# Kernel optimization log

Hardware: AMD Instinct MI355X
Metric: run time of the kernel (lower is better)

Reference implementation:

```python
import jax, jax.numpy as jnp
import numpy as np

K = 7          # neighborhood kernel size (7x7)
NH = 8         # num heads


def _nbr_idx(n):
    # NATTEN-style clamped windows: window start = clip(i - K//2, 0, n-K)
    pos = jnp.arange(n)
    start = jnp.clip(pos - K // 2, 0, n - K)          # (n,)
    idx = start[:, None] + jnp.arange(K)[None, :]     # (n, K) absolute key positions
    rel = idx - pos[:, None] + (K - 1)                # (n, K) in [0, 2K-2] for rpb lookup
    return idx, rel


def _forward(x, w_qkv, b_qkv, rpb, w_proj, b_proj, w_fc1, b_fc1, w_fc2, b_fc2):
    B, C, H, W = x.shape
    hd = C // NH
    scale = hd ** -0.5

    # ---- neighborhood attention (norm0 = Identity) ----
    xp = jnp.transpose(x, (0, 2, 3, 1))                           # (B,H,W,C)
    qkv = xp @ w_qkv + b_qkv                                      # (B,H,W,3C)
    qkv = qkv.reshape(B, H, W, 3, NH, hd)
    q = qkv[:, :, :, 0] * scale                                   # (B,H,W,nh,hd)
    k = qkv[:, :, :, 1]
    v = qkv[:, :, :, 2]

    idx_h, rel_h = _nbr_idx(H)                                    # (H,K)
    idx_w, rel_w = _nbr_idx(W)                                    # (W,K)

    # gather 7x7 neighborhoods: (B,H,K,W,K,nh,hd)
    k_nbr = k[:, idx_h][:, :, :, idx_w]
    v_nbr = v[:, idx_h][:, :, :, idx_w]

    # attention logits: (B,H,W,nh,K,K)
    attn = jnp.einsum('bxynd,bxiyjnd->bxynij', q, k_nbr)
    # relative positional bias: rpb (nh, 2K-1, 2K-1) -> (nh,H,K,W,K)
    bias = rpb[:, rel_h][:, :, :, rel_w]                          # (nh,H,K,W,K)
    attn = attn + jnp.transpose(bias, (1, 3, 0, 2, 4))[None]      # (B,H,W,nh,K,K)

    attn = jax.nn.softmax(attn.reshape(B, H, W, NH, K * K), axis=-1)
    attn = attn.reshape(B, H, W, NH, K, K)

    out = jnp.einsum('bxynij,bxiyjnd->bxynd', attn, v_nbr)        # (B,H,W,nh,hd)
    out = out.reshape(B, H, W, C) @ w_proj + b_proj               # (B,H,W,C)
    x1 = jnp.transpose(out, (0, 3, 1, 2)) + x                     # residual skip0

    # ---- MLP (1x1-conv style, channels-first; norm1 = Identity) ----
    h = jnp.einsum('bchw,cf->bfhw', x1, w_fc1) + b_fc1[None, :, None, None]
    h = jax.nn.gelu(h, approximate=False)                         # torch nn.GELU (erf)
    y = jnp.einsum('bfhw,fc->bchw', h, w_fc2) + b_fc2[None, :, None, None]
    return y + x1                                                 # residual skip1


def setup_inputs() -> dict:
    key = jax.random.key(0)
    B, C, H, W = 1, 256, 64, 128
    hid = int(C * 2.0)
    ks = jax.random.split(key, 8)
    s = 0.02
    return {
        'x': jax.random.normal(ks[0], (B, C, H, W), jnp.float32),
        'w_qkv': jax.random.normal(ks[1], (C, 3 * C), jnp.float32) * s,
        'b_qkv': jnp.zeros((3 * C,), jnp.float32),
        'rpb': jax.random.normal(ks[2], (NH, 2 * K - 1, 2 * K - 1), jnp.float32) * s,
        'w_proj': jax.random.normal(ks[3], (C, C), jnp.float32) * s,
        'b_proj': jnp.zeros((C,), jnp.float32),
        'w_fc1': jax.random.normal(ks[4], (C, hid), jnp.float32) * s,
        'b_fc1': jnp.zeros((hid,), jnp.float32),
        'w_fc2': jax.random.normal(ks[5], (hid, C), jnp.float32) * s,
        'b_fc2': jnp.zeros((C,), jnp.float32),
    }


def reference(x, w_qkv, b_qkv, rpb, w_proj, b_proj, w_fc1, b_fc1, w_fc2, b_fc2):
    return _forward(x, w_qkv, b_qkv, rpb, w_proj, b_proj, w_fc1, b_fc1, w_fc2, b_fc2)
```

## Files before the change

### kernel.cpp

```cpp
#include <hip/hip_runtime.h>

typedef unsigned short ushort;
typedef short bf16x8 __attribute__((ext_vector_type(8)));
typedef float f32x4 __attribute__((ext_vector_type(4)));

static __device__ __forceinline__ ushort f2b(float f) {
  unsigned u = __builtin_bit_cast(unsigned, f);
  u = (u + 0x7fffu + ((u >> 16) & 1u)) >> 16;
  return (ushort)u;
}
static __device__ __forceinline__ float b2f(ushort b) {
  return __builtin_bit_cast(float, (unsigned)b << 16);
}

static __device__ __forceinline__ void gll16(const ushort* g, ushort* l) {
  __builtin_amdgcn_global_load_lds(
      (const __attribute__((address_space(1))) void*)g,
      (__attribute__((address_space(3))) void*)l, 16, 0, 0);
}

__global__ __launch_bounds__(256) void prep_kernel(
    const float* __restrict__ x,
    const float* __restrict__ w_qkv, const float* __restrict__ w_proj,
    const float* __restrict__ w_fc1, const float* __restrict__ w_fc2,
    ushort* __restrict__ xb, ushort* __restrict__ wqkvT,
    ushort* __restrict__ wprojT, ushort* __restrict__ wfc1T,
    ushort* __restrict__ wfc2T)
{
  __shared__ float tile[32][33];
  int t = blockIdx.x;
  const float* src; ushort* dst; int R, Nc, r0, c0;
  if (t < 2048)              { src = x;      dst = xb;     R = 256; Nc = 8192; r0 = (t >> 8) * 32; c0 = (t & 255) * 32; }
  else if ((t -= 2048) < 192){ src = w_qkv;  dst = wqkvT;  R = 256; Nc = 768;  r0 = (t / 24) * 32; c0 = (t % 24) * 32; }
  else if ((t -= 192) < 64)  { src = w_proj; dst = wprojT; R = 256; Nc = 256;  r0 = (t / 8) * 32;  c0 = (t % 8) * 32; }
  else if ((t -= 64) < 128)  { src = w_fc1;  dst = wfc1T;  R = 256; Nc = 512;  r0 = (t / 16) * 32; c0 = (t % 16) * 32; }
  else           { t -= 128;   src = w_fc2;  dst = wfc2T;  R = 512; Nc = 256;  r0 = (t / 8) * 32;  c0 = (t % 8) * 32; }

  const int tx = threadIdx.x & 31, ty = threadIdx.x >> 5;
  #pragma unroll
  for (int i = 0; i < 4; i++)
    tile[ty + i * 8][tx] = src[(size_t)(r0 + ty + i * 8) * Nc + c0 + tx];
  __syncthreads();
  #pragma unroll
  for (int i = 0; i < 4; i++)
    dst[(size_t)(c0 + ty + i * 8) * R + r0 + tx] = f2b(tile[tx][ty + i * 8]);
}

template<int EPI, int KD>
__global__ __launch_bounds__(256) void gemm_mfma(
    const ushort* __restrict__ A, const ushort* __restrict__ Bt,
    const float* __restrict__ bias, const float* __restrict__ R,
    const ushort* __restrict__ RS,
    void* __restrict__ C0, void* __restrict__ C1,
    int M, int N)
{
  __shared__ __attribute__((aligned(16))) ushort As[64 * 128];
  __shared__ __attribute__((aligned(16))) ushort Bs[64 * 128];

  const int bm = blockIdx.y * 64;
  const int bn = blockIdx.x * 64;
  const int t  = threadIdx.x;
  const int w    = t >> 6;
  const int lane = t & 63;
  const int wm = (w & 1) * 32;
  const int wn = (w >> 1) * 32;
  const int lm = lane & 15;
  const int kq = lane >> 4;

  const int rl  = lane >> 4;
  const int cbx = (lane & 15) << 4;
  const int xr  = (lm & 7) << 4;

  f32x4 acc[2][2] = {};

  #pragma unroll
  for (int k0 = 0; k0 < KD; k0 += 128) {
    #pragma unroll
    for (int s = 0; s < 4; s++) {
      const int c = w * 4 + s;
      const int r = c * 4 + rl;
      const int off = (cbx ^ ((r & 7) << 4)) >> 1;
      gll16(A  + (size_t)(bm + r) * KD + k0 + off, As + c * 512);
      gll16(Bt + (size_t)(bn + r) * KD + k0 + off, Bs + c * 512);
    }
    __syncthreads();

    #pragma unroll
    for (int ks = 0; ks < 4; ks++) {
      const int kb = ks * 64 + (kq << 4);
      const int cs = kb ^ xr;
      bf16x8 a0 = *(const bf16x8*)((const char*)As + (wm + lm)      * 256 + cs);
      bf16x8 a1 = *(const bf16x8*)((const char*)As + (wm + 16 + lm) * 256 + cs);
      bf16x8 b0 = *(const bf16x8*)((const char*)Bs + (wn + lm)      * 256 + cs);
      bf16x8 b1 = *(const bf16x8*)((const char*)Bs + (wn + 16 + lm) * 256 + cs);
      acc[0][0] = __builtin_amdgcn_mfma_f32_16x16x32_bf16(a0, b0, acc[0][0], 0, 0, 0);
      acc[0][1] = __builtin_amdgcn_mfma_f32_16x16x32_bf16(a0, b1, acc[0][1], 0, 0, 0);
      acc[1][0] = __builtin_amdgcn_mfma_f32_16x16x32_bf16(a1, b0, acc[1][0], 0, 0, 0);
      acc[1][1] = __builtin_amdgcn_mfma_f32_16x16x32_bf16(a1, b1, acc[1][1], 0, 0, 0);
    }
    __syncthreads();
  }

  #pragma unroll
  for (int ti = 0; ti < 2; ti++) {
    #pragma unroll
    for (int tj = 0; tj < 2; tj++) {
      const int n  = bn + wn + tj * 16 + lm;
      const int m0 = bm + wm + ti * 16 + kq * 4;
      if (EPI == 3) {
        float4 v;
        float* vp = &v.x;
        #pragma unroll
        for (int r = 0; r < 4; r++)
          vp[r] = acc[ti][tj][r] + bias[n] + b2f(RS[(size_t)(m0 + r) * 256 + n]);
        *(float4*)((float*)C0 + (size_t)n * M + m0) = v;
      } else if (EPI == 0) {
        if (n < 512) {
          #pragma unroll
          for (int r = 0; r < 4; r++)
            ((ushort*)C0)[(size_t)(m0 + r) * N + n] = f2b(acc[ti][tj][r] + bias[n]);
        } else {
          ushort4 st;
          st.x = f2b(acc[ti][tj][0] + bias[n]);
          st.y = f2b(acc[ti][tj][1] + bias[n]);
          st.z = f2b(acc[ti][tj][2] + bias[n]);
          st.w = f2b(acc[ti][tj][3] + bias[n]);
          *(ushort4*)((ushort*)C1 + (size_t)(n - 512) * 8192 + m0) = st;
        }
      } else {
        #pragma unroll
        for (int r = 0; r < 4; r++) {
          const int m = m0 + r;
          float v = acc[ti][tj][r] + bias[n];
          if (EPI == 1) {
            v += R[(size_t)n * M + m];
            ((ushort*)C0)[(size_t)m * 256 + n] = f2b(v);
          } else {
            v = 0.5f * v * (1.0f + erff(v * 0.70710678118f));
            ((ushort*)C0)[(size_t)m * N + n] = f2b(v);
          }
        }
      }
    }
  }
}

__global__ __launch_bounds__(256, 4) void natt_mfma(
    const ushort* __restrict__ qkv, const ushort* __restrict__ vT,
    const float* __restrict__ rpb, ushort* __restrict__ att)
{
  __shared__ __attribute__((aligned(16))) ushort Plds[4][7][16][40];
  __shared__ float Rlds[4][176];

  const int w    = threadIdx.x >> 6;
  const int lane = threadIdx.x & 63;
  const int l  = lane & 15;
  const int q  = lane >> 4;
  const int tile = blockIdx.x;
  const int n    = blockIdx.y * 4 + w;
  const int ph  = tile >> 3;
  const int pw0 = (tile & 7) << 4;
  const int p0  = ph * 128 + pw0;

  int sh = ph - 3;  sh = sh < 0 ? 0 : (sh > 57 ? 57 : sh);
  int sb = pw0 - 3; sb = sb < 0 ? 0 : sb;
  const int sba = sb & ~7;

  const float L2E = 1.44269504f;
  for (int idx = lane; idx < 169; idx += 64)
    Rlds[w][idx] = rpb[n * 169 + idx] * L2E;

  bf16x8 qf = *(const bf16x8*)(qkv + (size_t)(p0 + l) * 768 + n * 32 + q * 8);

  const float KSC = 0.17677669529663689f * 1.44269504f;
  const int relh0 = sh - ph + 6;
  float rsum[4] = {0.f, 0.f, 0.f, 0.f};

  #pragma unroll
  for (int h = 0; h < 2; h++) {
    f32x4 s[7] = {};
    #pragma unroll
    for (int i = 0; i < 7; i++) {
      const int rowp = (sh + i) * 128;
      int jc = sba + h * 16 + l;
      jc = jc > 127 ? 127 : jc;
      bf16x8 kf = *(const bf16x8*)(qkv + (size_t)(rowp + jc) * 768 + 256 + n * 32 + q * 8);
      s[i] = __builtin_amdgcn_mfma_f32_16x16x32_bf16(qf, kf, s[i], 0, 0, 0);
    }
    #pragma unroll
    for (int r = 0; r < 4; r++) {
      const int pw = pw0 + q * 4 + r;
      int sw = pw - 3; sw = sw < 0 ? 0 : (sw > 121 ? 121 : sw);
      const int jc = sba + h * 16 + l;
      const bool valid = (unsigned)(jc - sw) <= 6u;
      int relw = jc - pw + 6;
      relw = relw < 0 ? 0 : (relw > 12 ? 12 : relw);
      #pragma unroll
      for (int i = 0; i < 7; i++) {
        float b = Rlds[w][(relh0 + i) * 13 + relw];
        float v = s[i][r] * KSC + b;
        v = valid ? v : -1e30f;
        float e = exp2f(v);
        rsum[r] += e;
        Plds[w][i][q * 4 + r][h * 16 + l] = f2b(e);
      }
    }
  }

  #pragma unroll
  for (int r = 0; r < 4; r++) {
    rsum[r] += __shfl_xor(rsum[r], 1);
    rsum[r] += __shfl_xor(rsum[r], 2);
    rsum[r] += __shfl_xor(rsum[r], 4);
    rsum[r] += __shfl_xor(rsum[r], 8);
  }

  f32x4 o[2] = {};
  #pragma unroll
  for (int i = 0; i < 7; i++) {
    bf16x8 pf = *(const bf16x8*)(&Plds[w][i][l][q * 8]);
    const int rowp = (sh + i) * 128;
    #pragma unroll
    for (int dh = 0; dh < 2; dh++) {
      bf16x8 vf = *(const bf16x8*)(vT + (size_t)(n * 32 + dh * 16 + l) * 8192
                                      + rowp + sba + q * 8);
      o[dh] = __builtin_amdgcn_mfma_f32_16x16x32_bf16(pf, vf, o[dh], 0, 0, 0);
    }
  }

  #pragma unroll
  for (int r = 0; r < 4; r++) {
    const float inv = 1.0f / rsum[r];
    #pragma unroll
    for (int dh = 0; dh < 2; dh++)
      att[(size_t)(p0 + q * 4 + r) * 256 + n * 32 + dh * 16 + l] = f2b(o[dh][r] * inv);
  }
}

extern "C" void kernel_launch(void* const* d_in, const int* in_sizes, int n_in,
                              void* d_out, int out_size, void* d_ws, size_t ws_size,
                              hipStream_t stream)
{
  const float* x      = (const float*)d_in[0];
  const float* w_qkv  = (const float*)d_in[1];
  const float* b_qkv  = (const float*)d_in[2];
  const float* rpb    = (const float*)d_in[3];
  const float* w_proj = (const float*)d_in[4];
  const float* b_proj = (const float*)d_in[5];
  const float* w_fc1  = (const float*)d_in[6];
  const float* b_fc1  = (const float*)d_in[7];
  const float* w_fc2  = (const float*)d_in[8];
  const float* b_fc2  = (const float*)d_in[9];
  float* out = (float*)d_out;

  const int M = 8192;
  char* ws = (char*)d_ws;
  ushort* xb     = (ushort*)(ws);
  ushort* qkv    = (ushort*)(ws + 4194304);
  ushort* x1b    = (ushort*)(ws + 16777216);
  ushort* wqkvT  = (ushort*)(ws + 20971520);
  ushort* wprojT = (ushort*)(ws + 21364736);
  ushort* wfc1T  = (ushort*)(ws + 21495808);
  ushort* wfc2T  = (ushort*)(ws + 21757952);
  ushort* vT     = (ushort*)(ws + 22020096);
  ushort* att = xb;
  ushort* h   = qkv;

  dim3 blk(256);

  prep_kernel<<<dim3(2560), blk, 0, stream>>>(
      x, w_qkv, w_proj, w_fc1, w_fc2, xb, wqkvT, wprojT, wfc1T, wfc2T);

  gemm_mfma<0, 256><<<dim3(768 / 64, M / 64), blk, 0, stream>>>(
      xb, wqkvT, b_qkv, nullptr, nullptr, qkv, vT, M, 768);

  natt_mfma<<<dim3(512, 2), blk, 0, stream>>>(qkv, vT, rpb, att);

  gemm_mfma<1, 256><<<dim3(256 / 64, M / 64), blk, 0, stream>>>(
      att, wprojT, b_proj, x, nullptr, x1b, nullptr, M, 256);

  gemm_mfma<2, 256><<<dim3(512 / 64, M / 64), blk, 0, stream>>>(
      x1b, wfc1T, b_fc1, nullptr, nullptr, h, nullptr, M, 512);

  gemm_mfma<3, 512><<<dim3(256 / 64, M / 64), blk, 0, stream>>>(
      h, wfc2T, b_fc2, nullptr, x1b, out, nullptr, M, 256);
}
```

Before: 133.2 us.

## Fuse proj, fc1 GELU and fc2 GEMMs into one shared-memory MLP kernel

Replaces the three separate GEMM launches for the output projection, fc1+GELU and fc2 with a single kernel that processes 32-row tiles. It keeps the x1 residual and the hidden activations in LDS. This removes global-memory round trips for the intermediates and two kernel launches. In exchange, each block reloads all weights, loads are not double-buffered, and the grid is only 256 large blocks, which limits occupancy and latency hiding.

```diff
diff --git a/kernel.cpp b/kernel.cpp
--- a/kernel.cpp
+++ b/kernel.cpp
@@ -107,14 +107,7 @@
     for (int tj = 0; tj < 2; tj++) {
       const int n  = bn + wn + tj * 16 + lm;
       const int m0 = bm + wm + ti * 16 + kq * 4;
-      if (EPI == 3) {
-        float4 v;
-        float* vp = &v.x;
-        #pragma unroll
-        for (int r = 0; r < 4; r++)
-          vp[r] = acc[ti][tj][r] + bias[n] + b2f(RS[(size_t)(m0 + r) * 256 + n]);
-        *(float4*)((float*)C0 + (size_t)n * M + m0) = v;
-      } else if (EPI == 0) {
+      if (EPI == 0) {
         if (n < 512) {
           #pragma unroll
           for (int r = 0; r < 4; r++)
@@ -127,19 +120,6 @@
           st.w = f2b(acc[ti][tj][3] + bias[n]);
           *(ushort4*)((ushort*)C1 + (size_t)(n - 512) * 8192 + m0) = st;
         }
-      } else {
-        #pragma unroll
-        for (int r = 0; r < 4; r++) {
-          const int m = m0 + r;
-          float v = acc[ti][tj][r] + bias[n];
-          if (EPI == 1) {
-            v += R[(size_t)n * M + m];
-            ((ushort*)C0)[(size_t)m * 256 + n] = f2b(v);
-          } else {
-            v = 0.5f * v * (1.0f + erff(v * 0.70710678118f));
-            ((ushort*)C0)[(size_t)m * N + n] = f2b(v);
-          }
-        }
       }
     }
   }
@@ -234,6 +214,155 @@
     #pragma unroll
     for (int dh = 0; dh < 2; dh++)
       att[(size_t)(p0 + q * 4 + r) * 256 + n * 32 + dh * 16 + l] = f2b(o[dh][r] * inv);
+  }
+}
+
+__global__ __launch_bounds__(512) void mlp_fused(
+    const ushort* __restrict__ att, const ushort* __restrict__ wprojT,
+    const ushort* __restrict__ wfc1T, const ushort* __restrict__ wfc2T,
+    const float* __restrict__ b_proj, const float* __restrict__ b_fc1,
+    const float* __restrict__ b_fc2, const float* __restrict__ xres,
+    float* __restrict__ out)
+{
+  __shared__ __attribute__((aligned(16))) ushort As[32 * 128];
+  __shared__ __attribute__((aligned(16))) ushort Bs[256 * 128];
+  __shared__ __attribute__((aligned(16))) ushort X1[32 * 256];
+  __shared__ __attribute__((aligned(16))) ushort Hs[32 * 256];
+
+  const int bm   = blockIdx.x * 32;
+  const int t    = threadIdx.x;
+  const int w    = t >> 6;
+  const int lane = t & 63;
+  const int lm   = lane & 15;
+  const int kq   = lane >> 4;
+  const int wm   = (w & 1) * 16;
+  const int wn   = (w >> 1) * 64;
+
+  const int rl  = lane >> 4;
+  const int swl = (lane & 15) << 3;
+
+  f32x4 acc_o[4] = {};
+
+  {
+    f32x4 acc_p[4] = {};
+    #pragma unroll
+    for (int kt = 0; kt < 2; kt++) {
+      {
+        const int m = w * 4 + rl;
+        gll16(att + (size_t)(bm + m) * 256 + kt * 128 + (swl ^ ((m & 7) << 3)),
+              As + w * 512);
+      }
+      #pragma unroll
+      for (int s = 0; s < 8; s++) {
+        const int c = w * 8 + s;
+        const int n = c * 4 + rl;
+        gll16(wprojT + (size_t)n * 256 + kt * 128 + (swl ^ ((n & 7) << 3)),
+              Bs + c * 512);
+      }
+      __syncthreads();
+      #pragma unroll
+      for (int ks = 0; ks < 4; ks++) {
+        const int kc = ks * 32 + kq * 8;
+        const int ar = wm + lm;
+        bf16x8 a = *(const bf16x8*)(&As[ar * 128 + (kc ^ ((ar & 7) << 3))]);
+        #pragma unroll
+        for (int tj = 0; tj < 4; tj++) {
+          const int n = wn + tj * 16 + lm;
+          bf16x8 b = *(const bf16x8*)(&Bs[n * 128 + (kc ^ ((n & 7) << 3))]);
+          acc_p[tj] = __builtin_amdgcn_mfma_f32_16x16x32_bf16(a, b, acc_p[tj], 0, 0, 0);
+        }
+      }
+      __syncthreads();
+    }
+    #pragma unroll
+    for (int tj = 0; tj < 4; tj++) {
+      const int n = wn + tj * 16 + lm;
+      #pragma unroll
+      for (int r = 0; r < 4; r++) {
+        const int m = wm + kq * 4 + r;
+        float v = acc_p[tj][r] + b_proj[n] + xres[(size_t)n * 8192 + bm + m];
+        X1[m * 256 + n] = f2b(v);
+      }
+    }
+    __syncthreads();
+  }
+
+  #pragma unroll
+  for (int hf = 0; hf < 2; hf++) {
+    f32x4 acc_h[4] = {};
+    #pragma unroll
+    for (int kt = 0; kt < 2; kt++) {
+      #pragma unroll
+      for (int s = 0; s < 8; s++) {
+        const int c = w * 8 + s;
+        const int n = c * 4 + rl;
+        gll16(wfc1T + (size_t)(hf * 256 + n) * 256 + kt * 128 + (swl ^ ((n & 7) << 3)),
+              Bs + c * 512);
+      }
+      __syncthreads();
+      #pragma unroll
+      for (int ks = 0; ks < 4; ks++) {
+        const int kc = ks * 32 + kq * 8;
+        const int ar = wm + lm;
+        bf16x8 a = *(const bf16x8*)(&X1[ar * 256 + kt * 128 + kc]);
+        #pragma unroll
+        for (int tj = 0; tj < 4; tj++) {
+          const int n = wn + tj * 16 + lm;
+          bf16x8 b = *(const bf16x8*)(&Bs[n * 128 + (kc ^ ((n & 7) << 3))]);
+          acc_h[tj] = __builtin_amdgcn_mfma_f32_16x16x32_bf16(a, b, acc_h[tj], 0, 0, 0);
+        }
+      }
+      __syncthreads();
+    }
+    #pragma unroll
+    for (int tj = 0; tj < 4; tj++) {
+      const int n = wn + tj * 16 + lm;
+      #pragma unroll
+      for (int r = 0; r < 4; r++) {
+        const int m = wm + kq * 4 + r;
+        float v = acc_h[tj][r] + b_fc1[hf * 256 + n];
+        v = 0.5f * v * (1.0f + erff(v * 0.70710678118f));
+        Hs[m * 256 + n] = f2b(v);
+      }
+    }
+    __syncthreads();
+
+    #pragma unroll
+    for (int kt = 0; kt < 2; kt++) {
+      #pragma unroll
+      for (int s = 0; s < 8; s++) {
+        const int c = w * 8 + s;
+        const int n = c * 4 + rl;
+        gll16(wfc2T + (size_t)n * 512 + hf * 256 + kt * 128 + (swl ^ ((n & 7) << 3)),
+              Bs + c * 512);
+      }
+      __syncthreads();
+      #pragma unroll
+      for (int ks = 0; ks < 4; ks++) {
+        const int kc = ks * 32 + kq * 8;
+        const int ar = wm + lm;
+        bf16x8 a = *(const bf16x8*)(&Hs[ar * 256 + kt * 128 + kc]);
+        #pragma unroll
+        for (int tj = 0; tj < 4; tj++) {
+          const int n = wn + tj * 16 + lm;
+          bf16x8 b = *(const bf16x8*)(&Bs[n * 128 + (kc ^ ((n & 7) << 3))]);
+          acc_o[tj] = __builtin_amdgcn_mfma_f32_16x16x32_bf16(a, b, acc_o[tj], 0, 0, 0);
+        }
+      }
+      __syncthreads();
+    }
+  }
+
+  #pragma unroll
+  for (int tj = 0; tj < 4; tj++) {
+    const int n  = wn + tj * 16 + lm;
+    const int m0 = wm + kq * 4;
+    float4 v;
+    float* vp = &v.x;
+    #pragma unroll
+    for (int r = 0; r < 4; r++)
+      vp[r] = acc_o[tj][r] + b_fc2[n] + b2f(X1[(m0 + r) * 256 + n]);
+    *(float4*)(out + (size_t)n * 8192 + bm + m0) = v;
   }
 }
 
@@ -257,14 +386,12 @@
   char* ws = (char*)d_ws;
   ushort* xb     = (ushort*)(ws);
   ushort* qkv    = (ushort*)(ws + 4194304);
-  ushort* x1b    = (ushort*)(ws + 16777216);
   ushort* wqkvT  = (ushort*)(ws + 20971520);
   ushort* wprojT = (ushort*)(ws + 21364736);
   ushort* wfc1T  = (ushort*)(ws + 21495808);
   ushort* wfc2T  = (ushort*)(ws + 21757952);
   ushort* vT     = (ushort*)(ws + 22020096);
   ushort* att = xb;
-  ushort* h   = qkv;
 
   dim3 blk(256);
 
@@ -276,12 +403,6 @@
 
   natt_mfma<<<dim3(512, 2), blk, 0, stream>>>(qkv, vT, rpb, att);
 
-  gemm_mfma<1, 256><<<dim3(256 / 64, M / 64), blk, 0, stream>>>(
-      att, wprojT, b_proj, x, nullptr, x1b, nullptr, M, 256);
-
-  gemm_mfma<2, 256><<<dim3(512 / 64, M / 64), blk, 0, stream>>>(
-      x1b, wfc1T, b_fc1, nullptr, nullptr, h, nullptr, M, 512);
-
-  gemm_mfma<3, 512><<<dim3(256 / 64, M / 64), blk, 0, stream>>>(
-      h, wfc2T, b_fc2, nullptr, x1b, out, nullptr, M, 256);
-}
+  mlp_fused<<<dim3(256), dim3(512), 0, stream>>>(
+      att, wprojT, wfc1T, wfc2T, b_proj, b_fc1, b_fc2, x, out);
+}
```

New measurement: 132.7 us. No clear change (-0.4%).

## Fuse projection, FC1+GELU and FC2 into one kernel with LDS intermediates

Applied to the files above, without the earlier changes.

Replaces the three separate GEMM launches (proj+residual, fc1+GELU, fc2+residual) with a single kernel. Each block handles 16 rows and keeps x1 and the hidden activations in swizzled shared memory, so neither goes to global memory and two launches disappear. In exchange, B operands are read straight from global memory with no LDS staging or reuse across blocks, only 512 blocks of 16 rows are launched, and the hidden dimension is processed in two halves with extra barriers.

```diff
diff --git a/kernel.cpp b/kernel.cpp
--- a/kernel.cpp
+++ b/kernel.cpp
@@ -107,14 +107,7 @@
     for (int tj = 0; tj < 2; tj++) {
       const int n  = bn + wn + tj * 16 + lm;
       const int m0 = bm + wm + ti * 16 + kq * 4;
-      if (EPI == 3) {
-        float4 v;
-        float* vp = &v.x;
-        #pragma unroll
-        for (int r = 0; r < 4; r++)
-          vp[r] = acc[ti][tj][r] + bias[n] + b2f(RS[(size_t)(m0 + r) * 256 + n]);
-        *(float4*)((float*)C0 + (size_t)n * M + m0) = v;
-      } else if (EPI == 0) {
+      if (EPI == 0) {
         if (n < 512) {
           #pragma unroll
           for (int r = 0; r < 4; r++)
@@ -127,19 +120,6 @@
           st.w = f2b(acc[ti][tj][3] + bias[n]);
           *(ushort4*)((ushort*)C1 + (size_t)(n - 512) * 8192 + m0) = st;
         }
-      } else {
-        #pragma unroll
-        for (int r = 0; r < 4; r++) {
-          const int m = m0 + r;
-          float v = acc[ti][tj][r] + bias[n];
-          if (EPI == 1) {
-            v += R[(size_t)n * M + m];
-            ((ushort*)C0)[(size_t)m * 256 + n] = f2b(v);
-          } else {
-            v = 0.5f * v * (1.0f + erff(v * 0.70710678118f));
-            ((ushort*)C0)[(size_t)m * N + n] = f2b(v);
-          }
-        }
       }
     }
   }
@@ -234,6 +214,110 @@
     #pragma unroll
     for (int dh = 0; dh < 2; dh++)
       att[(size_t)(p0 + q * 4 + r) * 256 + n * 32 + dh * 16 + l] = f2b(o[dh][r] * inv);
+  }
+}
+
+__global__ __launch_bounds__(512, 4) void mlp_fused(
+    const ushort* __restrict__ att, const ushort* __restrict__ wprojT,
+    const ushort* __restrict__ wfc1T, const ushort* __restrict__ wfc2T,
+    const float* __restrict__ b_proj, const float* __restrict__ b_fc1,
+    const float* __restrict__ b_fc2, const float* __restrict__ xres,
+    float* __restrict__ out)
+{
+  __shared__ __attribute__((aligned(16))) ushort X1[16 * 256];
+  __shared__ __attribute__((aligned(16))) ushort Hs[16 * 256];
+
+  const int bm   = blockIdx.x * 16;
+  const int w    = threadIdx.x >> 6;
+  const int lane = threadIdx.x & 63;
+  const int lm   = lane & 15;
+  const int kq   = lane >> 4;
+  const int wn   = w * 32;
+
+  {
+    f32x4 accp[2] = {};
+    #pragma unroll
+    for (int kk = 0; kk < 8; kk++) {
+      const int ko = kk * 32 + kq * 8;
+      bf16x8 a = *(const bf16x8*)(att + (size_t)(bm + lm) * 256 + ko);
+      #pragma unroll
+      for (int tj = 0; tj < 2; tj++) {
+        const int n = wn + tj * 16 + lm;
+        bf16x8 b = *(const bf16x8*)(wprojT + (size_t)n * 256 + ko);
+        accp[tj] = __builtin_amdgcn_mfma_f32_16x16x32_bf16(a, b, accp[tj], 0, 0, 0);
+      }
+    }
+    #pragma unroll
+    for (int tj = 0; tj < 2; tj++) {
+      const int n = wn + tj * 16 + lm;
+      const float bp = b_proj[n];
+      float4 xr = *(const float4*)(xres + (size_t)n * 8192 + bm + kq * 4);
+      const float* xp = &xr.x;
+      #pragma unroll
+      for (int r = 0; r < 4; r++) {
+        const int m = kq * 4 + r;
+        X1[m * 256 + (n ^ ((m & 7) << 3))] = f2b(accp[tj][r] + bp + xp[r]);
+      }
+    }
+  }
+  __syncthreads();
+
+  f32x4 acco[2] = {};
+  #pragma unroll
+  for (int hf = 0; hf < 2; hf++) {
+    f32x4 acch[2] = {};
+    #pragma unroll
+    for (int kk = 0; kk < 8; kk++) {
+      const int ko = kk * 32 + kq * 8;
+      bf16x8 a = *(const bf16x8*)(&X1[lm * 256 + (ko ^ ((lm & 7) << 3))]);
+      #pragma unroll
+      for (int tj = 0; tj < 2; tj++) {
+        const int n = wn + tj * 16 + lm;
+        bf16x8 b = *(const bf16x8*)(wfc1T + (size_t)(hf * 256 + n) * 256 + ko);
+        acch[tj] = __builtin_amdgcn_mfma_f32_16x16x32_bf16(a, b, acch[tj], 0, 0, 0);
+      }
+    }
+    #pragma unroll
+    for (int tj = 0; tj < 2; tj++) {
+      const int n = wn + tj * 16 + lm;
+      const float b1 = b_fc1[hf * 256 + n];
+      #pragma unroll
+      for (int r = 0; r < 4; r++) {
+        const int m = kq * 4 + r;
+        float v = acch[tj][r] + b1;
+        v = 0.5f * v * (1.0f + erff(v * 0.70710678118f));
+        Hs[m * 256 + (n ^ ((m & 7) << 3))] = f2b(v);
+      }
+    }
+    __syncthreads();
+
+    #pragma unroll
+    for (int kk = 0; kk < 8; kk++) {
+      const int ko = kk * 32 + kq * 8;
+      bf16x8 a = *(const bf16x8*)(&Hs[lm * 256 + (ko ^ ((lm & 7) << 3))]);
+      #pragma unroll
+      for (int tj = 0; tj < 2; tj++) {
+        const int n = wn + tj * 16 + lm;
+        bf16x8 b = *(const bf16x8*)(wfc2T + (size_t)n * 512 + hf * 256 + ko);
+        acco[tj] = __builtin_amdgcn_mfma_f32_16x16x32_bf16(a, b, acco[tj], 0, 0, 0);
+      }
+    }
+    __syncthreads();
+  }
+
+  #pragma unroll
+  for (int tj = 0; tj < 2; tj++) {
+    const int n  = wn + tj * 16 + lm;
+    const int m0 = kq * 4;
+    const float b2 = b_fc2[n];
+    float4 v;
+    float* vp = &v.x;
+    #pragma unroll
+    for (int r = 0; r < 4; r++) {
+      const int m = m0 + r;
+      vp[r] = acco[tj][r] + b2 + b2f(X1[m * 256 + (n ^ ((m & 7) << 3))]);
+    }
+    *(float4*)(out + (size_t)n * 8192 + bm + m0) = v;
   }
 }
 
@@ -257,14 +341,12 @@
   char* ws = (char*)d_ws;
   ushort* xb     = (ushort*)(ws);
   ushort* qkv    = (ushort*)(ws + 4194304);
-  ushort* x1b    = (ushort*)(ws + 16777216);
   ushort* wqkvT  = (ushort*)(ws + 20971520);
   ushort* wprojT = (ushort*)(ws + 21364736);
   ushort* wfc1T  = (ushort*)(ws + 21495808);
   ushort* wfc2T  = (ushort*)(ws + 21757952);
   ushort* vT     = (ushort*)(ws + 22020096);
   ushort* att = xb;
-  ushort* h   = qkv;
 
   dim3 blk(256);
 
@@ -276,12 +358,6 @@
 
   natt_mfma<<<dim3(512, 2), blk, 0, stream>>>(qkv, vT, rpb, att);
 
-  gemm_mfma<1, 256><<<dim3(256 / 64, M / 64), blk, 0, stream>>>(
-      att, wprojT, b_proj, x, nullptr, x1b, nullptr, M, 256);
-
-  gemm_mfma<2, 256><<<dim3(512 / 64, M / 64), blk, 0, stream>>>(
-      x1b, wfc1T, b_fc1, nullptr, nullptr, h, nullptr, M, 512);
-
-  gemm_mfma<3, 512><<<dim3(256 / 64, M / 64), blk, 0, stream>>>(
-      h, wfc2T, b_fc2, nullptr, x1b, out, nullptr, M, 256);
-}
+  mlp_fused<<<dim3(512), dim3(512), 0, stream>>>(
+      att, wprojT, wfc1T, wfc2T, b_proj, b_fc1, b_fc2, x, out);
+}
```

New measurement: 151.2 us. +13.5%, slower.

## Multi-buffer GEMM LDS stages to overlap global loads with MFMA compute

Applied to the files above, without the earlier changes.

The GEMM kernel now keeps up to three LDS buffers per operand. It issues the global-to-LDS loads for later K steps ahead of time, using explicit vmcnt waits and barriers instead of a sync before and after each K step. This aims to hide global load latency behind the MFMA work and to remove one barrier per iteration. In exchange, LDS use per block grows from 32KB to 64KB, or 96KB for the K=512 GEMM, which may reduce the number of blocks resident per CU.

```diff
diff --git a/kernel.cpp b/kernel.cpp
--- a/kernel.cpp
+++ b/kernel.cpp
@@ -18,6 +18,11 @@
       (const __attribute__((address_space(1))) void*)g,
       (__attribute__((address_space(3))) void*)l, 16, 0, 0);
 }
+
+#define SWAIT(N)                                                            \
+  asm volatile("s_waitcnt vmcnt(" #N ")" ::: "memory");                     \
+  __builtin_amdgcn_s_barrier();                                             \
+  __builtin_amdgcn_sched_barrier(0)
 
 __global__ __launch_bounds__(256) void prep_kernel(
     const float* __restrict__ x,
@@ -47,15 +52,17 @@
 }
 
 template<int EPI, int KD>
-__global__ __launch_bounds__(256) void gemm_mfma(
+__global__ __launch_bounds__(256) void gemm_stream(
     const ushort* __restrict__ A, const ushort* __restrict__ Bt,
     const float* __restrict__ bias, const float* __restrict__ R,
     const ushort* __restrict__ RS,
     void* __restrict__ C0, void* __restrict__ C1,
     int M, int N)
 {
-  __shared__ __attribute__((aligned(16))) ushort As[64 * 128];
-  __shared__ __attribute__((aligned(16))) ushort Bs[64 * 128];
+  constexpr int S  = KD / 128;
+  constexpr int NB = (S < 3) ? S : 3;
+  __shared__ __attribute__((aligned(16))) ushort As[NB][64 * 128];
+  __shared__ __attribute__((aligned(16))) ushort Bs[NB][64 * 128];
 
   const int bm = blockIdx.y * 64;
   const int bn = blockIdx.x * 64;
@@ -73,32 +80,40 @@
 
   f32x4 acc[2][2] = {};
 
-  #pragma unroll
-  for (int k0 = 0; k0 < KD; k0 += 128) {
-    #pragma unroll
-    for (int s = 0; s < 4; s++) {
-      const int c = w * 4 + s;
+  auto stage = [&](int slot, int step) {
+    #pragma unroll
+    for (int j = 0; j < 4; j++) {
+      const int c = w * 4 + j;
       const int r = c * 4 + rl;
       const int off = (cbx ^ ((r & 7) << 4)) >> 1;
-      gll16(A  + (size_t)(bm + r) * KD + k0 + off, As + c * 512);
-      gll16(Bt + (size_t)(bn + r) * KD + k0 + off, Bs + c * 512);
-    }
-    __syncthreads();
-
+      gll16(A  + (size_t)(bm + r) * KD + step * 128 + off, &As[slot][c * 512]);
+      gll16(Bt + (size_t)(bn + r) * KD + step * 128 + off, &Bs[slot][c * 512]);
+    }
+  };
+  auto compute = [&](int slot) {
     #pragma unroll
     for (int ks = 0; ks < 4; ks++) {
       const int kb = ks * 64 + (kq << 4);
       const int cs = kb ^ xr;
-      bf16x8 a0 = *(const bf16x8*)((const char*)As + (wm + lm)      * 256 + cs);
-      bf16x8 a1 = *(const bf16x8*)((const char*)As + (wm + 16 + lm) * 256 + cs);
-      bf16x8 b0 = *(const bf16x8*)((const char*)Bs + (wn + lm)      * 256 + cs);
-      bf16x8 b1 = *(const bf16x8*)((const char*)Bs + (wn + 16 + lm) * 256 + cs);
+      bf16x8 a0 = *(const bf16x8*)((const char*)&As[slot][0] + (wm + lm)      * 256 + cs);
+      bf16x8 a1 = *(const bf16x8*)((const char*)&As[slot][0] + (wm + 16 + lm) * 256 + cs);
+      bf16x8 b0 = *(const bf16x8*)((const char*)&Bs[slot][0] + (wn + lm)      * 256 + cs);
+      bf16x8 b1 = *(const bf16x8*)((const char*)&Bs[slot][0] + (wn + 16 + lm) * 256 + cs);
       acc[0][0] = __builtin_amdgcn_mfma_f32_16x16x32_bf16(a0, b0, acc[0][0], 0, 0, 0);
       acc[0][1] = __builtin_amdgcn_mfma_f32_16x16x32_bf16(a0, b1, acc[0][1], 0, 0, 0);
       acc[1][0] = __builtin_amdgcn_mfma_f32_16x16x32_bf16(a1, b0, acc[1][0], 0, 0, 0);
       acc[1][1] = __builtin_amdgcn_mfma_f32_16x16x32_bf16(a1, b1, acc[1][1], 0, 0, 0);
     }
-    __syncthreads();
+  };
+
+  stage(0, 0);
+  if (S > 1) stage(1, 1);
+
+  #pragma unroll
+  for (int s = 0; s < S; s++) {
+    if (s < S - 1) { SWAIT(8); } else { SWAIT(0); }
+    if (s + 2 < S) stage((s + 2) % NB, s + 2);
+    compute(s % NB);
   }
 
   #pragma unroll
@@ -271,17 +286,17 @@
   prep_kernel<<<dim3(2560), blk, 0, stream>>>(
       x, w_qkv, w_proj, w_fc1, w_fc2, xb, wqkvT, wprojT, wfc1T, wfc2T);
 
-  gemm_mfma<0, 256><<<dim3(768 / 64, M / 64), blk, 0, stream>>>(
+  gemm_stream<0, 256><<<dim3(768 / 64, M / 64), blk, 0, stream>>>(
       xb, wqkvT, b_qkv, nullptr, nullptr, qkv, vT, M, 768);
 
   natt_mfma<<<dim3(512, 2), blk, 0, stream>>>(qkv, vT, rpb, att);
 
-  gemm_mfma<1, 256><<<dim3(256 / 64, M / 64), blk, 0, stream>>>(
+  gemm_stream<1, 256><<<dim3(256 / 64, M / 64), blk, 0, stream>>>(
       att, wprojT, b_proj, x, nullptr, x1b, nullptr, M, 256);
 
-  gemm_mfma<2, 256><<<dim3(512 / 64, M / 64), blk, 0, stream>>>(
+  gemm_stream<2, 256><<<dim3(512 / 64, M / 64), blk, 0, stream>>>(
       x1b, wfc1T, b_fc1, nullptr, nullptr, h, nullptr, M, 512);
 
-  gemm_mfma<3, 512><<<dim3(256 / 64, M / 64), blk, 0, stream>>>(
+  gemm_stream<3, 512><<<dim3(256 / 64, M / 64), blk, 0, stream>>>(
       h, wfc2T, b_fc2, nullptr, x1b, out, nullptr, M, 256);
 }
```

After: 136.9 us. 2.7% more time.
